# Performance work log

Measured on AMD Instinct MI355X. Metric: run time of the kernel, lower is better.

## Reference

```python
import jax, jax.numpy as jnp
import numpy as np
from jax.scipy.special import logsumexp

TAU = 1.0
N_ITERS = 20
D = 1024
B = 65536


def setup_inputs() -> dict:
    key = jax.random.key(0)
    k1, k2 = jax.random.split(key)
    embeddings = jax.random.normal(k1, (B, D), dtype=jnp.float32)
    log_scores = jax.random.normal(k2, (D, D), dtype=jnp.float32) * 0.01
    return {"embeddings": embeddings, "log_scores": log_scores}


def _sinkhorn(log_alpha):
    # 20 alternating row/column logsumexp normalizations on a (d, d) matrix
    def body(_, la):
        la = la - logsumexp(la, axis=-1, keepdims=True)  # row normalize
        la = la - logsumexp(la, axis=-2, keepdims=True)  # col normalize
        return la
    log_alpha = jax.lax.fori_loop(0, N_ITERS, body, log_alpha)
    return jnp.exp(log_alpha)


def reference(embeddings, log_scores):
    P = _sinkhorn(log_scores / TAU)           # (d, d) approx doubly stochastic
    # (P @ embeddings.T).T == embeddings @ P.T
    return embeddings @ P.T                   # (B, d)
```

## Files before the change

### kernel.cpp

```cpp
#include <hip/hip_runtime.h>
#include <hip/hip_bf16.h>

#define D_DIM 1024
#define NITER 20

typedef float f32x4 __attribute__((ext_vector_type(4)));
typedef __bf16 bf16x4 __attribute__((ext_vector_type(4)));
typedef __bf16 bf16x8 __attribute__((ext_vector_type(8)));

__global__ __launch_bounds__(1024)
void prep_exp_transpose(const float* __restrict__ ls, float* __restrict__ Mm,
                        float* __restrict__ Mt) {
    __shared__ float tile[64][65];
    const int tx = threadIdx.x, ty = threadIdx.y;
    const int bx = blockIdx.x * 64, by = blockIdx.y * 64;
#pragma unroll
    for (int k = 0; k < 64; k += 16) {
        int r = by + ty + k, c = bx + tx;
        float v = expf(ls[r * D_DIM + c]);
        Mm[r * D_DIM + c] = v;
        tile[ty + k][tx] = v;
    }
    __syncthreads();
#pragma unroll
    for (int k = 0; k < 64; k += 16) {
        int r = bx + ty + k, c = by + tx;
        Mt[r * D_DIM + c] = tile[tx][ty + k];
    }
}

__global__ void init_u(float* u) { u[threadIdx.x] = 1.0f; }

__global__ __launch_bounds__(256)
void matvec_recip(const float* __restrict__ A, const float* __restrict__ x,
                  float* __restrict__ y) {
    const int wave = threadIdx.x >> 6, lane = threadIdx.x & 63;
    const int row = blockIdx.x * 4 + wave;
    const f32x4* Ar = (const f32x4*)(A + row * D_DIM);
    const f32x4* xr = (const f32x4*)x;
    float s = 0.f;
#pragma unroll
    for (int it = 0; it < 4; ++it) {
        f32x4 a = Ar[lane + it * 64];
        f32x4 b = xr[lane + it * 64];
        s += a.x * b.x + a.y * b.y + a.z * b.z + a.w * b.w;
    }
#pragma unroll
    for (int off = 32; off > 0; off >>= 1) s += __shfl_down(s, off, 64);
    if (lane == 0) y[row] = 1.0f / s;
}

__global__ __launch_bounds__(256)
void finalize_P(const float* __restrict__ Mm, const float* __restrict__ r,
                const float* __restrict__ u, __bf16* __restrict__ P) {
    const int i = blockIdx.x;
    const int t = threadIdx.x;
    const float ri = r[i];
    f32x4 m = ((const f32x4*)(Mm + i * D_DIM))[t];
    f32x4 uu = ((const f32x4*)u)[t];
    bf16x4 o;
    o[0] = (__bf16)(m.x * ri * uu.x);
    o[1] = (__bf16)(m.y * ri * uu.y);
    o[2] = (__bf16)(m.z * ri * uu.z);
    o[3] = (__bf16)(m.w * ri * uu.w);
    ((bf16x4*)(P + i * D_DIM))[t] = o;
}

#define BM 128
#define BN 128
#define BK 32

__global__ __launch_bounds__(256)
void gemm_a32_bt16(const float* __restrict__ A, const __bf16* __restrict__ Bt,
                   float* __restrict__ C, int Msz, int Nsz, int Ksz) {
    __shared__ __bf16 As[BM * BK];
    __shared__ __bf16 Bs[BN * BK];
    const int tid = threadIdx.x;
    const int wave = tid >> 6, lane = tid & 63;
    const int wm = wave >> 1, wn = wave & 1;
    const int quad = lane >> 4, l16 = lane & 15;
    const int m0 = blockIdx.y * BM, n0 = blockIdx.x * BN;

    f32x4 acc[4][4] = {};

    for (int k0 = 0; k0 < Ksz; k0 += BK) {
        __syncthreads();
#pragma unroll
        for (int it = 0; it < 4; ++it) {
            int idx = tid + it * 256;
            int row = idx >> 3, kq = idx & 7;
            f32x4 v = *(const f32x4*)(A + (size_t)(m0 + row) * Ksz + k0 + kq * 4);
            bf16x4 b;
            b[0] = (__bf16)v.x; b[1] = (__bf16)v.y;
            b[2] = (__bf16)v.z; b[3] = (__bf16)v.w;
            *(bf16x4*)(&As[row * BK + kq * 4]) = b;
        }
#pragma unroll
        for (int q = 0; q < 2; ++q) {
            int t8 = wave * 2 + q;
            int nrow = t8 * 16 + (lane >> 2);
            const __bf16* g = Bt + (size_t)(n0 + nrow) * Ksz + k0 + (lane & 3) * 8;
            __bf16* l = Bs + t8 * 512;
            __builtin_amdgcn_global_load_lds(
                (const __attribute__((address_space(1))) void*)g,
                (__attribute__((address_space(3))) void*)l, 16, 0, 0);
        }
        __syncthreads();

        bf16x8 af[4], bfr[4];
#pragma unroll
        for (int a = 0; a < 4; ++a)
            af[a] = *(const bf16x8*)(&As[(wm * 64 + a * 16 + l16) * BK + quad * 8]);
#pragma unroll
        for (int b = 0; b < 4; ++b)
            bfr[b] = *(const bf16x8*)(&Bs[(wn * 64 + b * 16 + l16) * BK + quad * 8]);
#pragma unroll
        for (int a = 0; a < 4; ++a)
#pragma unroll
            for (int b = 0; b < 4; ++b)
                acc[a][b] = __builtin_amdgcn_mfma_f32_16x16x32_bf16(
                    af[a], bfr[b], acc[a][b], 0, 0, 0);
    }

#pragma unroll
    for (int a = 0; a < 4; ++a) {
        int mg = m0 + wm * 64 + a * 16 + quad * 4;
#pragma unroll
        for (int b = 0; b < 4; ++b) {
            int ng = n0 + wn * 64 + b * 16 + l16;
#pragma unroll
            for (int v = 0; v < 4; ++v)
                C[(size_t)(mg + v) * Nsz + ng] = acc[a][b][v];
        }
    }
}

extern "C" void kernel_launch(void* const* d_in, const int* in_sizes, int n_in,
                              void* d_out, int out_size, void* d_ws, size_t ws_size,
                              hipStream_t stream) {
    const float* emb = (const float*)d_in[0];
    const float* ls  = (const float*)d_in[1];
    float* out = (float*)d_out;
    char* ws = (char*)d_ws;

    float* Mm  = (float*)ws;
    float* Mt  = (float*)(ws + (4u << 20));
    float* r   = (float*)(ws + (8u << 20));
    float* u   = (float*)(ws + (8u << 20) + 4096);
    __bf16* P  = (__bf16*)(ws + (8u << 20) + 8192);

    const int B = in_sizes[0] / D_DIM;

    prep_exp_transpose<<<dim3(16, 16), dim3(64, 16), 0, stream>>>(ls, Mm, Mt);
    init_u<<<1, D_DIM, 0, stream>>>(u);
    for (int it = 0; it < NITER; ++it) {
        matvec_recip<<<D_DIM / 4, 256, 0, stream>>>(Mm, u, r);
        matvec_recip<<<D_DIM / 4, 256, 0, stream>>>(Mt, r, u);
    }
    finalize_P<<<D_DIM, 256, 0, stream>>>(Mm, r, u, P);
    gemm_a32_bt16<<<dim3(D_DIM / BN, B / BM), 256, 0, stream>>>(
        emb, P, out, B, D_DIM, D_DIM);
}
```

Baseline: 742.2 us.

## Swizzle GEMM LDS layout, remap tiles per XCD, fold u init into prep

Applies an XOR swizzle to the A and B shared-memory tiles, both on the write side (register stores and global_load_lds source addresses) and on the MFMA fragment reads, to cut LDS bank conflicts. Replaces the 2D grid with a 1D grid whose block index is remapped so each XCD processes groups of M-tiles across all N-tiles, aiming for better L2 reuse of the embedding rows. Also initializes u inside the prep kernel, removing one launch. The swizzle has to match exactly between the global_load_lds lane mapping and the reads, which is easy to get wrong.

New measurement: 709.5 us. 4.4% less time.

```diff
diff --git a/kernel.cpp b/kernel.cpp
--- a/kernel.cpp
+++ b/kernel.cpp
@@ -10,7 +10,7 @@
 
 __global__ __launch_bounds__(1024)
 void prep_exp_transpose(const float* __restrict__ ls, float* __restrict__ Mm,
-                        float* __restrict__ Mt) {
+                        float* __restrict__ Mt, float* __restrict__ u) {
     __shared__ float tile[64][65];
     const int tx = threadIdx.x, ty = threadIdx.y;
     const int bx = blockIdx.x * 64, by = blockIdx.y * 64;
@@ -21,6 +21,7 @@
         Mm[r * D_DIM + c] = v;
         tile[ty + k][tx] = v;
     }
+    if (blockIdx.x == 0 && blockIdx.y == 0) u[ty * 64 + tx] = 1.0f;
     __syncthreads();
 #pragma unroll
     for (int k = 0; k < 64; k += 16) {
@@ -28,8 +29,6 @@
         Mt[r * D_DIM + c] = tile[tx][ty + k];
     }
 }
-
-__global__ void init_u(float* u) { u[threadIdx.x] = 1.0f; }
 
 __global__ __launch_bounds__(256)
 void matvec_recip(const float* __restrict__ A, const float* __restrict__ x,
@@ -79,27 +78,33 @@
     const int wave = tid >> 6, lane = tid & 63;
     const int wm = wave >> 1, wn = wave & 1;
     const int quad = lane >> 4, l16 = lane & 15;
-    const int m0 = blockIdx.y * BM, n0 = blockIdx.x * BN;
+    const int f = blockIdx.x;
+    const int xcd = f & 7, s = f >> 3;
+    const int m0 = (((s >> 3) << 3) | xcd) * BM;
+    const int n0 = (s & 7) * BN;
+    const int sR = (l16 >> 1) & 3;
 
     f32x4 acc[4][4] = {};
 
     for (int k0 = 0; k0 < Ksz; k0 += BK) {
         __syncthreads();
 #pragma unroll
-        for (int it = 0; it < 4; ++it) {
-            int idx = tid + it * 256;
-            int row = idx >> 3, kq = idx & 7;
-            f32x4 v = *(const f32x4*)(A + (size_t)(m0 + row) * Ksz + k0 + kq * 4);
+        for (int itc = 0; itc < 4; ++itc) {
+            int idx = tid + itc * 256;
+            int arow = idx >> 3, kq = idx & 7;
+            f32x4 v = *(const f32x4*)(A + (size_t)(m0 + arow) * Ksz + k0 + kq * 4);
             bf16x4 b;
             b[0] = (__bf16)v.x; b[1] = (__bf16)v.y;
             b[2] = (__bf16)v.z; b[3] = (__bf16)v.w;
-            *(bf16x4*)(&As[row * BK + kq * 4]) = b;
+            int slot = (kq >> 1) ^ ((arow >> 1) & 3);
+            *(bf16x4*)(&As[arow * BK + slot * 8 + (kq & 1) * 4]) = b;
         }
 #pragma unroll
         for (int q = 0; q < 2; ++q) {
             int t8 = wave * 2 + q;
             int nrow = t8 * 16 + (lane >> 2);
-            const __bf16* g = Bt + (size_t)(n0 + nrow) * Ksz + k0 + (lane & 3) * 8;
+            int kb = (lane & 3) ^ ((lane >> 3) & 3);
+            const __bf16* g = Bt + (size_t)(n0 + nrow) * Ksz + k0 + kb * 8;
             __bf16* l = Bs + t8 * 512;
             __builtin_amdgcn_global_load_lds(
                 (const __attribute__((address_space(1))) void*)g,
@@ -109,11 +114,15 @@
 
         bf16x8 af[4], bfr[4];
 #pragma unroll
-        for (int a = 0; a < 4; ++a)
-            af[a] = *(const bf16x8*)(&As[(wm * 64 + a * 16 + l16) * BK + quad * 8]);
+        for (int a = 0; a < 4; ++a) {
+            int arow = wm * 64 + a * 16 + l16;
+            af[a] = *(const bf16x8*)(&As[arow * BK + (quad ^ sR) * 8]);
+        }
 #pragma unroll
-        for (int b = 0; b < 4; ++b)
-            bfr[b] = *(const bf16x8*)(&Bs[(wn * 64 + b * 16 + l16) * BK + quad * 8]);
+        for (int b = 0; b < 4; ++b) {
+            int brow = wn * 64 + b * 16 + l16;
+            bfr[b] = *(const bf16x8*)(&Bs[brow * BK + (quad ^ sR) * 8]);
+        }
 #pragma unroll
         for (int a = 0; a < 4; ++a)
 #pragma unroll
@@ -151,13 +160,12 @@
 
     const int B = in_sizes[0] / D_DIM;
 
-    prep_exp_transpose<<<dim3(16, 16), dim3(64, 16), 0, stream>>>(ls, Mm, Mt);
-    init_u<<<1, D_DIM, 0, stream>>>(u);
+    prep_exp_transpose<<<dim3(16, 16), dim3(64, 16), 0, stream>>>(ls, Mm, Mt, u);
     for (int it = 0; it < NITER; ++it) {
         matvec_recip<<<D_DIM / 4, 256, 0, stream>>>(Mm, u, r);
         matvec_recip<<<D_DIM / 4, 256, 0, stream>>>(Mt, r, u);
     }
     finalize_P<<<D_DIM, 256, 0, stream>>>(Mm, r, u, P);
-    gemm_a32_bt16<<<dim3(D_DIM / BN, B / BM), 256, 0, stream>>>(
+    gemm_a32_bt16<<<dim3((B / BM) * (D_DIM / BN)), 256, 0, stream>>>(
         emb, P, out, B, D_DIM, D_DIM);
 }
```
